# Kernel optimization log

Hardware: AMD Instinct MI355X
Metric: run time of the kernel (lower is better)

The kernel has to match this reference:

```python
import jax, jax.numpy as jnp
import numpy as np

B, H, N, D = 16, 8, 256, 32


def setup_inputs() -> dict:
    key = jax.random.key(0)
    k1, k2, k3 = jax.random.split(key, 3)
    q = jax.random.normal(k1, (B, H, N, D), dtype=jnp.float32)
    k = jax.random.normal(k2, (B, H, N, D), dtype=jnp.float32)
    scale = jnp.ones((1,), dtype=jnp.float32)  # unused by the module
    mask = jnp.zeros((B, 1, N, N), dtype=bool)  # True == masked out
    # learned attention vector, xavier_uniform over (1, H, 1, 1, D)
    fan = 1 * H * 1 * 1 * D
    bound = float(np.sqrt(6.0 / (1 + D)))  # xavier for (..., D) param
    attention = jax.random.uniform(k3, (1, H, 1, 1, D), dtype=jnp.float32,
                                   minval=-bound, maxval=bound)
    return {"q": q, "k": k, "scale": scale, "mask": mask, "attention": attention}


def reference(q, k, scale, mask, attention):
    # summed: [B, H, Nq, Nk, D] via broadcast of q.unsqueeze(-2)+k.unsqueeze(-3)
    summed = q[:, :, :, None, :] + k[:, :, None, :, :]
    # GATv2 score: a^T * silu(q_i + k_j), reduced over head_dim
    scores = jnp.sum(jax.nn.silu(summed) * attention, axis=-1)  # [B, H, Nq, Nk]
    neg = jnp.finfo(scores.dtype).min
    scores_masked = jnp.where(mask, neg, scores)
    attn = jax.nn.softmax(scores_masked, axis=-1)
    return attn
```

## Files before the change

### kernel.cpp

```cpp
#include <hip/hip_runtime.h>
#include <stdint.h>
#include <stddef.h>

constexpr int Bc = 16, Hc = 8, Nc = 256, Dc = 32;
constexpr float LOG2E = 1.44269504088896340736f;

constexpr int    MF    = 10;
constexpr double PHALF = 9.7;
constexpr double LFIT  = 9.0;

constexpr double PI_ = 3.14159265358979323846;

constexpr double cexp_(double x) {
    int n = (int)(x >= 0 ? x + 0.5 : x - 0.5);
    double f = x - n, t = 1.0, s = 1.0;
    for (int i = 1; i <= 26; ++i) { t *= f / i; s += t; }
    const double E = 2.71828182845904523536;
    double en = 1.0, bb = n >= 0 ? E : 1.0 / E;
    int an = n < 0 ? -n : n;
    for (int i = 0; i < an; ++i) en *= bb;
    return s * en;
}
constexpr double creduce_(double x) {
    while (x >  PI_) x -= 2.0 * PI_;
    while (x < -PI_) x += 2.0 * PI_;
    return x;
}
constexpr double ccos_(double x0) {
    double x = creduce_(x0), x2 = x * x, t = 1.0, s = 1.0;
    for (int i = 1; i <= 16; ++i) { t *= -x2 / ((2.0*i - 1.0) * (2.0*i)); s += t; }
    return s;
}
constexpr double csin_(double x0) {
    double x = creduce_(x0), x2 = x * x, t = x, s = x;
    for (int i = 1; i <= 16; ++i) { t *= -x2 / ((2.0*i) * (2.0*i + 1.0)); s += t; }
    return s;
}
constexpr double Gfun_(double x) {
    double z = x < 0 ? -x : x;
    double e = cexp_(z);
    return 0.5 * z * ((e - 1.0) / (e + 1.0));
}
constexpr double csqrt_(double x) {
    if (x <= 0) return 0;
    double r = x > 1 ? x : 1;
    for (int i = 0; i < 40; ++i) r = 0.5 * (r + x / r);
    return r;
}

struct FitT { float tk[MF + 1]; float tq[MF + 1]; };

constexpr FitT lsFit_() {
    constexpr int NB = MF + 1;
    double A[NB][NB] = {}, bv[NB] = {};
    for (int p = 0; p < NB; ++p)
        for (int qq = 0; qq < NB; ++qq) {
            double wm = (p - qq) * PI_ / PHALF, wp = (p + qq) * PI_ / PHALF;
            double Sm = (p == qq)     ? LFIT : csin_(wm * LFIT) / wm;
            double Sp = (p + qq == 0) ? LFIT : csin_(wp * LFIT) / wp;
            A[p][qq] = 0.5 * (Sm + Sp);
        }
    constexpr int NS = 128;
    double hh = LFIT / NS, gx[NS + 1] = {};
    for (int i = 0; i <= NS; ++i) gx[i] = Gfun_(i * hh);
    for (int p = 0; p < NB; ++p) {
        double s = 0;
        for (int i = 0; i <= NS; ++i) {
            double wgt = (i == 0 || i == NS) ? 1.0 : ((i & 1) ? 4.0 : 2.0);
            s += wgt * gx[i] * ccos_(p * PI_ / PHALF * (i * hh));
        }
        bv[p] = s * hh / 3.0;
    }
    for (int p = 0; p < NB; ++p) A[p][p] += 1e-8 * LFIT;
    for (int col = 0; col < NB; ++col) {
        int piv = col; double best = A[col][col] < 0 ? -A[col][col] : A[col][col];
        for (int r = col + 1; r < NB; ++r) {
            double v = A[r][col] < 0 ? -A[r][col] : A[r][col];
            if (v > best) { best = v; piv = r; }
        }
        if (piv != col) {
            for (int cc = 0; cc < NB; ++cc) { double t = A[col][cc]; A[col][cc] = A[piv][cc]; A[piv][cc] = t; }
            double t = bv[col]; bv[col] = bv[piv]; bv[piv] = t;
        }
        for (int r = col + 1; r < NB; ++r) {
            double f = A[r][col] / A[col][col];
            for (int cc = col; cc < NB; ++cc) A[r][cc] -= f * A[col][cc];
            bv[r] -= f * bv[col];
        }
    }
    double c[NB] = {};
    for (int r = NB - 1; r >= 0; --r) {
        double s = bv[r];
        for (int cc = r + 1; cc < NB; ++cc) s -= A[r][cc] * c[cc];
        c[r] = s / A[r][r];
    }
    FitT f{};
    for (int m = 0; m <= MF; ++m) {
        double rt = csqrt_(c[m] < 0 ? -c[m] : c[m]);
        f.tk[m] = (float)rt;
        f.tq[m] = (float)(c[m] < 0 ? -rt : rt);
    }
    return f;
}
constexpr FitT CF = lsFit_();

typedef _Float16 half8  __attribute__((ext_vector_type(8)));
typedef float    f32x16 __attribute__((ext_vector_type(16)));

__device__ __forceinline__ uint32_t pkh_(float a, float b) {
    auto v = __builtin_amdgcn_cvt_pkrtz(a, b);
    uint32_t u; __builtin_memcpy(&u, &v, 4); return u;
}

constexpr int KB_  = Nc * 128;
constexpr int QB_  = 128 * 128;
constexpr int BUF  = KB_ + QB_;
constexpr int SRED_OFF = 2 * BUF;
constexpr int AKV_OFF  = SRED_OFF + 2048;
constexpr int SMEM     = AKV_OFF + 1024;

__global__ __launch_bounds__(512, 2) void gatv2_mfma_kernel(
    const float* __restrict__ q, const float* __restrict__ k,
    const uint8_t* __restrict__ mask, const float* __restrict__ att,
    float* __restrict__ out)
{
    extern __shared__ char smem[];
    float* sred = (float*)(smem + SRED_OFF);
    float* akv  = (float*)(smem + AKV_OFF);

    const int tid = threadIdx.x, lane = tid & 63, w = tid >> 6;
    const int bh = blockIdx.y, h = bh & 7, b = bh >> 3;
    const int iBlk = blockIdx.x * 128;
    const float invTwoP = (float)(1.0 / (2.0 * PHALF));

    const int dq = tid & 7, rw = tid >> 3;
    const float4 a4 = *(const float4*)(att + h * Dc + 4 * dq);
    const int swS = (dq ^ (rw & 7)) << 4;

    const float* kbase = k + (size_t)bh * Nc * Dc;
    float kc1[16], ks1[16], kcm[16], ksm[16];
    int offK[4];
#pragma unroll
    for (int it = 0; it < 4; ++it) {
        const int j = rw + it * 64;
        const float4 kv = *(const float4*)(kbase + j * Dc + 4 * dq);
        float part = a4.x * kv.x + a4.y * kv.y + a4.z * kv.z + a4.w * kv.w;
        part += __shfl_xor(part, 1, 64);
        part += __shfl_xor(part, 2, 64);
        part += __shfl_xor(part, 4, 64);
        if (dq == 0) akv[j] = part;
        const float rv[4] = { kv.x, kv.y, kv.z, kv.w };
#pragma unroll
        for (int c = 0; c < 4; ++c) {
            float r = __builtin_amdgcn_fractf(rv[c] * invTwoP);
            kc1[4*it+c] = __builtin_amdgcn_cosf(r);
            ks1[4*it+c] = __builtin_amdgcn_sinf(r);
            kcm[4*it+c] = kc1[4*it+c];
            ksm[4*it+c] = ks1[4*it+c];
        }
        offK[it] = j * 128 + swS;
    }
    const float* qbase = q + ((size_t)bh * Nc + iBlk) * Dc;
    float qc1[8], qs1[8], qcm[8], qsm[8];
    int offQ[2];
#pragma unroll
    for (int it = 0; it < 2; ++it) {
        const int iq = rw + it * 64;
        const float4 qv = *(const float4*)(qbase + iq * Dc + 4 * dq);
        const float rv[4] = { qv.x, qv.y, qv.z, qv.w };
#pragma unroll
        for (int c = 0; c < 4; ++c) {
            float r = __builtin_amdgcn_fractf(rv[c] * invTwoP);
            qc1[4*it+c] = __builtin_amdgcn_cosf(r);
            qs1[4*it+c] = __builtin_amdgcn_sinf(r);
            qcm[4*it+c] = qc1[4*it+c];
            qsm[4*it+c] = qs1[4*it+c];
        }
        offQ[it] = KB_ + iq * 128 + swS;
    }

    const int hi5 = lane >> 5, col = lane & 31;
    const int wi = w & 1, wj = w >> 1;
    const int baseA0 = KB_ + (wi * 64 + col) * 128, baseA1 = baseA0 + 32 * 128;
    const int baseB0 = (wj * 64 + col) * 128,       baseB1 = baseB0 + 32 * 128;
    const int sA = col & 7;

    f32x16 acc[2][2];
#pragma unroll
    for (int i2 = 0; i2 < 2; ++i2)
#pragma unroll
        for (int j2 = 0; j2 < 2; ++j2)
#pragma unroll
            for (int e = 0; e < 16; ++e) acc[i2][j2][e] = 0.0f;

    auto buildWrite = [&](int mN, int dstOff) {
        const float tk = CF.tk[mN];
        const float g0 = CF.tq[mN]*a4.x, g1 = CF.tq[mN]*a4.y;
        const float g2 = CF.tq[mN]*a4.z, g3 = CF.tq[mN]*a4.w;
#pragma unroll
        for (int it = 0; it < 4; ++it) {
            uint4 wv;
            wv.x = pkh_(tk * kcm[4*it+0], tk * ksm[4*it+0]);
            wv.y = pkh_(tk * kcm[4*it+1], tk * ksm[4*it+1]);
            wv.z = pkh_(tk * kcm[4*it+2], tk * ksm[4*it+2]);
            wv.w = pkh_(tk * kcm[4*it+3], tk * ksm[4*it+3]);
            *(uint4*)(smem + dstOff + offK[it]) = wv;
        }
#pragma unroll
        for (int it = 0; it < 2; ++it) {
            uint4 wv;
            wv.x = pkh_(g0 * qcm[4*it+0], -(g0 * qsm[4*it+0]));
            wv.y = pkh_(g1 * qcm[4*it+1], -(g1 * qsm[4*it+1]));
            wv.z = pkh_(g2 * qcm[4*it+2], -(g2 * qsm[4*it+2]));
            wv.w = pkh_(g3 * qcm[4*it+3], -(g3 * qsm[4*it+3]));
            *(uint4*)(smem + dstOff + offQ[it]) = wv;
        }
    };
    auto rotate = [&]() {
#pragma unroll
        for (int e = 0; e < 16; ++e) {
            float cn = fmaf(kc1[e], kcm[e], -(ks1[e] * ksm[e]));
            float sn = fmaf(ks1[e], kcm[e],   kc1[e] * ksm[e]);
            kcm[e] = cn; ksm[e] = sn;
        }
#pragma unroll
        for (int e = 0; e < 8; ++e) {
            float cn = fmaf(qc1[e], qcm[e], -(qs1[e] * qsm[e]));
            float sn = fmaf(qs1[e], qcm[e],   qc1[e] * qsm[e]);
            qcm[e] = cn; qsm[e] = sn;
        }
    };
    auto loadFrags = [&](int srcOff, int s, half8& A0, half8& A1,
                         half8& B0, half8& B1) {
        const int du = ((2 * s + hi5) ^ sA) << 4;
        A0 = *(const half8*)(smem + srcOff + baseA0 + du);
        A1 = *(const half8*)(smem + srcOff + baseA1 + du);
        B0 = *(const half8*)(smem + srcOff + baseB0 + du);
        B1 = *(const half8*)(smem + srcOff + baseB1 + du);
    };
    auto mfma4 = [&](half8 A0, half8 A1, half8 B0, half8 B1) {
        acc[0][0] = __builtin_amdgcn_mfma_f32_32x32x16_f16(A0, B0, acc[0][0], 0, 0, 0);
        acc[0][1] = __builtin_amdgcn_mfma_f32_32x32x16_f16(A0, B1, acc[0][1], 0, 0, 0);
        acc[1][0] = __builtin_amdgcn_mfma_f32_32x32x16_f16(A1, B0, acc[1][0], 0, 0, 0);
        acc[1][1] = __builtin_amdgcn_mfma_f32_32x32x16_f16(A1, B1, acc[1][1], 0, 0, 0);
    };

    buildWrite(1, 0);
    rotate();
    __syncthreads();
#pragma unroll
    for (int m = 1; m <= MF; ++m) {
        const int srcOff = ((m - 1) & 1) * BUF;
        const int dstOff = (m & 1) * BUF;
        half8 A0a, A1a, B0a, B1a, A0b, A1b, B0b, B1b;
        loadFrags(srcOff, 0, A0a, A1a, B0a, B1a);
        loadFrags(srcOff, 1, A0b, A1b, B0b, B1b);
        if (m < MF) { buildWrite(m + 1, dstOff); rotate(); }
        __builtin_amdgcn_s_setprio(1);
        mfma4(A0a, A1a, B0a, B1a);
        loadFrags(srcOff, 2, A0a, A1a, B0a, B1a);
        mfma4(A0b, A1b, B0b, B1b);
        loadFrags(srcOff, 3, A0b, A1b, B0b, B1b);
        mfma4(A0a, A1a, B0a, B1a);
        mfma4(A0b, A1b, B0b, B1b);
        __builtin_amdgcn_s_setprio(0);
        if (m < MF) __syncthreads();
    }

    constexpr float M0 = 24.0f;
    const int jB = wj * 64;
    const float akj0 = akv[jB + col], akj1 = akv[jB + 32 + col];
    const int iB = iBlk + wi * 64;

#pragma unroll
    for (int i2 = 0; i2 < 2; ++i2) {
        float v[16];
#pragma unroll
        for (int e = 0; e < 16; ++e) {
            const int rloc = (e & 3) + 8 * (e >> 2) + 4 * hi5;
            const int ig = iB + i2 * 32 + rloc;
            const uint8_t* mr = mask + ((size_t)(b * Nc + ig)) * Nc + jB + col;
            float v0 = fmaf(0.5f, akj0, acc[i2][0][e]);
            float v1 = fmaf(0.5f, akj1, acc[i2][1][e]);
            if (mr[0])  v0 = -1.0e30f;
            if (mr[32]) v1 = -1.0e30f;
            float p0 = __builtin_amdgcn_exp2f(__builtin_fminf((v0 - M0) * LOG2E, 80.0f));
            float p1 = __builtin_amdgcn_exp2f(__builtin_fminf((v1 - M0) * LOG2E, 80.0f));
            acc[i2][0][e] = p0;
            acc[i2][1][e] = p1;
            v[e] = p0 + p1;
        }
        float u8[8];
#pragma unroll
        for (int jj = 0; jj < 8; ++jj) {
            float mine = (col & 16) ? v[jj + 8] : v[jj];
            float send = (col & 16) ? v[jj]     : v[jj + 8];
            u8[jj] = mine + __shfl_xor(send, 16, 64);
        }
        float u4[4];
#pragma unroll
        for (int jj = 0; jj < 4; ++jj) {
            float mine = (col & 8) ? u8[jj + 4] : u8[jj];
            float send = (col & 8) ? u8[jj]     : u8[jj + 4];
            u4[jj] = mine + __shfl_xor(send, 8, 64);
        }
        float u2[2];
#pragma unroll
        for (int jj = 0; jj < 2; ++jj) {
            float mine = (col & 4) ? u2[0] * 0.0f + ((col & 4) ? u4[jj + 2] : u4[jj]) : u4[jj];
            (void)mine;
            float mn = (col & 4) ? u4[jj + 2] : u4[jj];
            float sd = (col & 4) ? u4[jj]     : u4[jj + 2];
            u2[jj] = mn + __shfl_xor(sd, 4, 64);
        }
        float t1;
        {
            float mn = (col & 2) ? u2[1] : u2[0];
            float sd = (col & 2) ? u2[0] : u2[1];
            t1 = mn + __shfl_xor(sd, 2, 64);
        }
        t1 += __shfl_xor(t1, 1, 64);
        {
            const int eL = ((col & 16) ? 8 : 0) + ((col & 8) ? 4 : 0)
                         + ((col & 4) ? 2 : 0) + ((col & 2) ? 1 : 0);
            const int rl = (eL & 3) + 8 * (eL >> 2) + 4 * hi5;
            if (!(col & 1)) sred[(wi * 64 + i2 * 32 + rl) * 4 + wj] = t1;
        }
    }
    __syncthreads();

    float* obase = out + (size_t)bh * Nc * Nc;
#pragma unroll
    for (int i2 = 0; i2 < 2; ++i2)
#pragma unroll
    for (int e = 0; e < 16; ++e) {
        const int rloc = (e & 3) + 8 * (e >> 2) + 4 * hi5;
        const int iL = wi * 64 + i2 * 32 + rloc;
        const int ig = iBlk + iL;
        const float4 tv = *(const float4*)(&sred[iL * 4]);
        const float inv = __builtin_amdgcn_rcpf(tv.x + tv.y + tv.z + tv.w);
        obase[(size_t)ig * Nc + jB + col]      = acc[i2][0][e] * inv;
        obase[(size_t)ig * Nc + jB + 32 + col] = acc[i2][1][e] * inv;
    }
}

extern "C" void kernel_launch(void* const* d_in, const int* in_sizes, int n_in,
                              void* d_out, int out_size, void* d_ws, size_t ws_size,
                              hipStream_t stream) {
    const float*   q    = (const float*)d_in[0];
    const float*   k    = (const float*)d_in[1];
    const uint8_t* mask = (const uint8_t*)d_in[3];
    const float*   att  = (const float*)d_in[4];
    float*         out  = (float*)d_out;

    (void)hipFuncSetAttribute((const void*)gatv2_mfma_kernel,
                              hipFuncAttributeMaxDynamicSharedMemorySize, SMEM);

    dim3 grid(2, Bc * Hc);
    dim3 block(512);
    gatv2_mfma_kernel<<<grid, block, SMEM, stream>>>(q, k, mask, att, out);
}
```

Baseline: 92.22 us.

## Build Q-side MFMA fragments in registers instead of staging through LDS

Each wave now computes its own A (query) fragments directly in registers. It recomputes cos/sin of m times the reduced phase per Fourier mode, instead of rotating and writing Q features to shared memory and reading them back. This removes the Q half of the LDS double buffer and its reads and writes, and folds the attention vector into the K side. In exchange each wave runs many more transcendental ops per mode (the same Q rows are recomputed by several waves) and holds more registers. The mask is now applied after the exp by zeroing the probability, which also decouples the mask loads from the exp.

After: 100.4 us. +8.8%, slower.

```diff
diff --git a/kernel.cpp b/kernel.cpp
--- a/kernel.cpp
+++ b/kernel.cpp
@@ -111,11 +111,13 @@
     auto v = __builtin_amdgcn_cvt_pkrtz(a, b);
     uint32_t u; __builtin_memcpy(&u, &v, 4); return u;
 }
+__device__ __forceinline__ half8 mk8_(uint32_t x, uint32_t y, uint32_t z, uint32_t w) {
+    uint4 u{x, y, z, w};
+    half8 h; __builtin_memcpy(&h, &u, 16); return h;
+}
 
 constexpr int KB_  = Nc * 128;
-constexpr int QB_  = 128 * 128;
-constexpr int BUF  = KB_ + QB_;
-constexpr int SRED_OFF = 2 * BUF;
+constexpr int SRED_OFF = 2 * KB_;
 constexpr int AKV_OFF  = SRED_OFF + 2048;
 constexpr int SMEM     = AKV_OFF + 1024;
 
@@ -160,31 +162,30 @@
         }
         offK[it] = j * 128 + swS;
     }
-    const float* qbase = q + ((size_t)bh * Nc + iBlk) * Dc;
-    float qc1[8], qs1[8], qcm[8], qsm[8];
-    int offQ[2];
-#pragma unroll
-    for (int it = 0; it < 2; ++it) {
-        const int iq = rw + it * 64;
-        const float4 qv = *(const float4*)(qbase + iq * Dc + 4 * dq);
-        const float rv[4] = { qv.x, qv.y, qv.z, qv.w };
-#pragma unroll
-        for (int c = 0; c < 4; ++c) {
-            float r = __builtin_amdgcn_fractf(rv[c] * invTwoP);
-            qc1[4*it+c] = __builtin_amdgcn_cosf(r);
-            qs1[4*it+c] = __builtin_amdgcn_sinf(r);
-            qcm[4*it+c] = qc1[4*it+c];
-            qsm[4*it+c] = qs1[4*it+c];
-        }
-        offQ[it] = KB_ + iq * 128 + swS;
-    }
 
     const int hi5 = lane >> 5, col = lane & 31;
     const int wi = w & 1, wj = w >> 1;
-    const int baseA0 = KB_ + (wi * 64 + col) * 128, baseA1 = baseA0 + 32 * 128;
-    const int baseB0 = (wj * 64 + col) * 128,       baseB1 = baseB0 + 32 * 128;
+    const int baseB0 = (wj * 64 + col) * 128, baseB1 = baseB0 + 32 * 128;
     const int sA = col & 7;
 
+    float r1A[32];
+    {
+        const float* qrow0 = q + ((size_t)bh * Nc + iBlk + wi * 64 + col) * Dc;
+#pragma unroll
+        for (int row = 0; row < 2; ++row) {
+            const float* qr = qrow0 + row * 32 * Dc;
+#pragma unroll
+            for (int s = 0; s < 4; ++s) {
+                const float4 qv = *(const float4*)(qr + 8 * s + 4 * hi5);
+                const float rv[4] = { qv.x, qv.y, qv.z, qv.w };
+#pragma unroll
+                for (int t = 0; t < 4; ++t)
+                    r1A[(row * 4 + s) * 4 + t] =
+                        __builtin_amdgcn_fractf(rv[t] * invTwoP);
+            }
+        }
+    }
+
     f32x16 acc[2][2];
 #pragma unroll
     for (int i2 = 0; i2 < 2; ++i2)
@@ -193,50 +194,42 @@
 #pragma unroll
             for (int e = 0; e < 16; ++e) acc[i2][j2][e] = 0.0f;
 
-    auto buildWrite = [&](int mN, int dstOff) {
-        const float tk = CF.tk[mN];
-        const float g0 = CF.tq[mN]*a4.x, g1 = CF.tq[mN]*a4.y;
-        const float g2 = CF.tq[mN]*a4.z, g3 = CF.tq[mN]*a4.w;
+    auto buildWriteK = [&](int mN, int dstOff) {
+        const float t0 = CF.tk[mN] * a4.x, t1 = CF.tk[mN] * a4.y;
+        const float t2 = CF.tk[mN] * a4.z, t3 = CF.tk[mN] * a4.w;
 #pragma unroll
         for (int it = 0; it < 4; ++it) {
             uint4 wv;
-            wv.x = pkh_(tk * kcm[4*it+0], tk * ksm[4*it+0]);
-            wv.y = pkh_(tk * kcm[4*it+1], tk * ksm[4*it+1]);
-            wv.z = pkh_(tk * kcm[4*it+2], tk * ksm[4*it+2]);
-            wv.w = pkh_(tk * kcm[4*it+3], tk * ksm[4*it+3]);
+            wv.x = pkh_(t0 * kcm[4*it+0], t0 * ksm[4*it+0]);
+            wv.y = pkh_(t1 * kcm[4*it+1], t1 * ksm[4*it+1]);
+            wv.z = pkh_(t2 * kcm[4*it+2], t2 * ksm[4*it+2]);
+            wv.w = pkh_(t3 * kcm[4*it+3], t3 * ksm[4*it+3]);
             *(uint4*)(smem + dstOff + offK[it]) = wv;
         }
-#pragma unroll
-        for (int it = 0; it < 2; ++it) {
-            uint4 wv;
-            wv.x = pkh_(g0 * qcm[4*it+0], -(g0 * qsm[4*it+0]));
-            wv.y = pkh_(g1 * qcm[4*it+1], -(g1 * qsm[4*it+1]));
-            wv.z = pkh_(g2 * qcm[4*it+2], -(g2 * qsm[4*it+2]));
-            wv.w = pkh_(g3 * qcm[4*it+3], -(g3 * qsm[4*it+3]));
-            *(uint4*)(smem + dstOff + offQ[it]) = wv;
-        }
-    };
-    auto rotate = [&]() {
+    };
+    auto rotateK = [&]() {
 #pragma unroll
         for (int e = 0; e < 16; ++e) {
             float cn = fmaf(kc1[e], kcm[e], -(ks1[e] * ksm[e]));
             float sn = fmaf(ks1[e], kcm[e],   kc1[e] * ksm[e]);
             kcm[e] = cn; ksm[e] = sn;
         }
-#pragma unroll
-        for (int e = 0; e < 8; ++e) {
-            float cn = fmaf(qc1[e], qcm[e], -(qs1[e] * qsm[e]));
-            float sn = fmaf(qs1[e], qcm[e],   qc1[e] * qsm[e]);
-            qcm[e] = cn; qsm[e] = sn;
-        }
-    };
-    auto loadFrags = [&](int srcOff, int s, half8& A0, half8& A1,
-                         half8& B0, half8& B1) {
+    };
+    auto loadB = [&](int srcOff, int s, half8& B0, half8& B1) {
         const int du = ((2 * s + hi5) ^ sA) << 4;
-        A0 = *(const half8*)(smem + srcOff + baseA0 + du);
-        A1 = *(const half8*)(smem + srcOff + baseA1 + du);
         B0 = *(const half8*)(smem + srcOff + baseB0 + du);
         B1 = *(const half8*)(smem + srcOff + baseB1 + du);
+    };
+    auto buildA = [&](float mf, float tq, int row, int s) -> half8 {
+        uint32_t u[4];
+#pragma unroll
+        for (int t = 0; t < 4; ++t) {
+            const float r = __builtin_amdgcn_fractf(mf * r1A[(row * 4 + s) * 4 + t]);
+            const float c = __builtin_amdgcn_cosf(r);
+            const float sn = __builtin_amdgcn_sinf(r);
+            u[t] = pkh_(tq * c, -(tq * sn));
+        }
+        return mk8_(u[0], u[1], u[2], u[3]);
     };
     auto mfma4 = [&](half8 A0, half8 A1, half8 B0, half8 B1) {
         acc[0][0] = __builtin_amdgcn_mfma_f32_32x32x16_f16(A0, B0, acc[0][0], 0, 0, 0);
@@ -245,24 +238,29 @@
         acc[1][1] = __builtin_amdgcn_mfma_f32_32x32x16_f16(A1, B1, acc[1][1], 0, 0, 0);
     };
 
-    buildWrite(1, 0);
-    rotate();
+    buildWriteK(1, 0);
+    rotateK();
     __syncthreads();
 #pragma unroll
     for (int m = 1; m <= MF; ++m) {
-        const int srcOff = ((m - 1) & 1) * BUF;
-        const int dstOff = (m & 1) * BUF;
-        half8 A0a, A1a, B0a, B1a, A0b, A1b, B0b, B1b;
-        loadFrags(srcOff, 0, A0a, A1a, B0a, B1a);
-        loadFrags(srcOff, 1, A0b, A1b, B0b, B1b);
-        if (m < MF) { buildWrite(m + 1, dstOff); rotate(); }
+        const int srcOff = ((m - 1) & 1) * KB_;
+        const int dstOff = (m & 1) * KB_;
+        half8 B0a, B1a, B0b, B1b;
+        loadB(srcOff, 0, B0a, B1a);
+        loadB(srcOff, 1, B0b, B1b);
+        if (m < MF) { buildWriteK(m + 1, dstOff); rotateK(); }
+        const float mf = (float)m, tq = CF.tq[m];
+        half8 A00 = buildA(mf, tq, 0, 0), A10 = buildA(mf, tq, 1, 0);
+        half8 A01 = buildA(mf, tq, 0, 1), A11 = buildA(mf, tq, 1, 1);
+        half8 A02 = buildA(mf, tq, 0, 2), A12 = buildA(mf, tq, 1, 2);
+        half8 A03 = buildA(mf, tq, 0, 3), A13 = buildA(mf, tq, 1, 3);
         __builtin_amdgcn_s_setprio(1);
-        mfma4(A0a, A1a, B0a, B1a);
-        loadFrags(srcOff, 2, A0a, A1a, B0a, B1a);
-        mfma4(A0b, A1b, B0b, B1b);
-        loadFrags(srcOff, 3, A0b, A1b, B0b, B1b);
-        mfma4(A0a, A1a, B0a, B1a);
-        mfma4(A0b, A1b, B0b, B1b);
+        mfma4(A00, A10, B0a, B1a);
+        loadB(srcOff, 2, B0a, B1a);
+        mfma4(A01, A11, B0b, B1b);
+        loadB(srcOff, 3, B0b, B1b);
+        mfma4(A02, A12, B0a, B1a);
+        mfma4(A03, A13, B0b, B1b);
         __builtin_amdgcn_s_setprio(0);
         if (m < MF) __syncthreads();
     }
@@ -280,12 +278,13 @@
             const int rloc = (e & 3) + 8 * (e >> 2) + 4 * hi5;
             const int ig = iB + i2 * 32 + rloc;
             const uint8_t* mr = mask + ((size_t)(b * Nc + ig)) * Nc + jB + col;
+            const uint8_t m0 = mr[0], m1 = mr[32];
             float v0 = fmaf(0.5f, akj0, acc[i2][0][e]);
             float v1 = fmaf(0.5f, akj1, acc[i2][1][e]);
-            if (mr[0])  v0 = -1.0e30f;
-            if (mr[32]) v1 = -1.0e30f;
             float p0 = __builtin_amdgcn_exp2f(__builtin_fminf((v0 - M0) * LOG2E, 80.0f));
             float p1 = __builtin_amdgcn_exp2f(__builtin_fminf((v1 - M0) * LOG2E, 80.0f));
+            if (m0) p0 = 0.0f;
+            if (m1) p1 = 0.0f;
             acc[i2][0][e] = p0;
             acc[i2][1][e] = p1;
             v[e] = p0 + p1;
@@ -293,22 +292,20 @@
         float u8[8];
 #pragma unroll
         for (int jj = 0; jj < 8; ++jj) {
-            float mine = (col & 16) ? v[jj + 8] : v[jj];
-            float send = (col & 16) ? v[jj]     : v[jj + 8];
-            u8[jj] = mine + __shfl_xor(send, 16, 64);
+            float mn = (col & 16) ? v[jj + 8] : v[jj];
+            float sd = (col & 16) ? v[jj]     : v[jj + 8];
+            u8[jj] = mn + __shfl_xor(sd, 16, 64);
         }
         float u4[4];
 #pragma unroll
         for (int jj = 0; jj < 4; ++jj) {
-            float mine = (col & 8) ? u8[jj + 4] : u8[jj];
-            float send = (col & 8) ? u8[jj]     : u8[jj + 4];
-            u4[jj] = mine + __shfl_xor(send, 8, 64);
+            float mn = (col & 8) ? u8[jj + 4] : u8[jj];
+            float sd = (col & 8) ? u8[jj]     : u8[jj + 4];
+            u4[jj] = mn + __shfl_xor(sd, 8, 64);
         }
         float u2[2];
 #pragma unroll
         for (int jj = 0; jj < 2; ++jj) {
-            float mine = (col & 4) ? u2[0] * 0.0f + ((col & 4) ? u4[jj + 2] : u4[jj]) : u4[jj];
-            (void)mine;
             float mn = (col & 4) ? u4[jj + 2] : u4[jj];
             float sd = (col & 4) ? u4[jj]     : u4[jj + 2];
             u2[jj] = mn + __shfl_xor(sd, 4, 64);
```
